# Performance work log

Hardware: AMD Instinct MI355X
Metric: run time of the kernel (lower is better)

Reference implementation:

```python
import jax, jax.numpy as jnp
import numpy as np

B, S, D, H = 4, 2048, 512, 4
HD = D // H
EPS = 1e-5


def layer_norm(x, gamma, beta):
    mu = jnp.mean(x, axis=-1, keepdims=True)
    var = jnp.mean(jnp.square(x - mu), axis=-1, keepdims=True)
    return (x - mu) * jax.lax.rsqrt(var + EPS) * gamma + beta


def setup_inputs() -> dict:
    key = jax.random.key(0)
    ks = jax.random.split(key, 16)
    s_in = 1.0 / np.sqrt(D)
    s_ex = 1.0 / np.sqrt(2 * D)
    return {
        "input_states": jax.random.normal(ks[0], (B, S, D), jnp.float32),
        "positions": jax.random.normal(ks[1], (B, S, 3), jnp.float32),
        "W_expand": jax.random.uniform(ks[2], (D, 2 * D), jnp.float32, -s_in, s_in),
        "b_expand": jax.random.uniform(ks[3], (2 * D,), jnp.float32, -s_in, s_in),
        "W_squeeze": jax.random.uniform(ks[4], (2 * D, D), jnp.float32, -s_ex, s_ex),
        "b_squeeze": jax.random.uniform(ks[5], (D,), jnp.float32, -s_ex, s_ex),
        "gamma": jnp.ones((D,), jnp.float32),
        "beta": jnp.zeros((D,), jnp.float32),
        "Wq": jax.random.uniform(ks[6], (D, D), jnp.float32, -s_in, s_in),
        "bq": jax.random.uniform(ks[7], (D,), jnp.float32, -s_in, s_in),
        "Wk": jax.random.uniform(ks[8], (D, D), jnp.float32, -s_in, s_in),
        "bk": jax.random.uniform(ks[9], (D,), jnp.float32, -s_in, s_in),
        "Wv": jax.random.uniform(ks[10], (D, D), jnp.float32, -s_in, s_in),
        "bv": jax.random.uniform(ks[11], (D,), jnp.float32, -s_in, s_in),
        "alpha": jnp.float32(0.1),
    }


def reference(input_states, positions, W_expand, b_expand, W_squeeze, b_squeeze,
              gamma, beta, Wq, bq, Wk, bk, Wv, bv, alpha):
    # FFN (expand -> relu -> squeeze) + residual + LayerNorm
    h = jax.nn.relu(input_states @ W_expand + b_expand)
    squeezed = h @ W_squeeze + b_squeeze
    se = layer_norm(input_states + squeezed, gamma, beta)

    # q/k/v projections, split heads: [B,H,S,HD]
    q = (se @ Wq + bq).reshape(B, S, H, HD).transpose(0, 2, 1, 3)
    k = (se @ Wk + bk).reshape(B, S, H, HD).transpose(0, 2, 1, 3)
    v = (se @ Wv + bv).reshape(B, S, H, HD).transpose(0, 2, 1, 3)

    scores = jnp.einsum('bhid,bhjd->bhij', q, k) / np.sqrt(HD)

    # squared pairwise distance bias: ||pi||^2 + ||pj||^2 - 2 pi.pj, broadcast over heads
    sq = jnp.sum(positions * positions, axis=-1)  # [B,S]
    dist2 = sq[:, :, None] + sq[:, None, :] - 2.0 * jnp.einsum('bic,bjc->bij', positions, positions)
    dist2 = jnp.maximum(dist2, 0.0)
    scores = scores - alpha * dist2[:, None, :, :]

    w = jax.nn.softmax(scores, axis=-1)
    ctx = jnp.einsum('bhij,bhjd->bhid', w, v)
    ctx = ctx.transpose(0, 2, 1, 3).reshape(B, S, D)

    # same LayerNorm params reused (self.norm applied twice in original)
    return layer_norm(se + ctx, gamma, beta)
```

## Files before the change

kernel.cpp:

```cpp
#include <hip/hip_runtime.h>

typedef __bf16 bf16_t;
typedef __attribute__((ext_vector_type(8))) __bf16 bf16x8;
typedef __attribute__((ext_vector_type(4))) __bf16 bf16x4;
typedef __attribute__((ext_vector_type(4))) float f32x4;
typedef __attribute__((ext_vector_type(16))) float f32x16;

constexpr int Bc = 4, Sc = 2048, Dc = 512, Hc = 4, HDc = 128;
constexpr int Mrows = Bc * Sc;

__device__ inline void gl2lds(const void* g, void* l) {
  __builtin_amdgcn_global_load_lds(
      (__attribute__((address_space(1))) void*)g,
      (__attribute__((address_space(3))) void*)l, 16, 0, 0);
}

__global__ __launch_bounds__(256) void prep_k(
    const float* __restrict__ X, bf16_t* __restrict__ xb,
    const float* __restrict__ We, bf16_t* __restrict__ wtE,
    const float* __restrict__ Ws, bf16_t* __restrict__ wtS,
    const float* __restrict__ Wq, const float* __restrict__ Wk,
    const float* __restrict__ Wv, bf16_t* __restrict__ wtQKV) {
  const int bid = blockIdx.x;
  if (bid < 2048) {
    const long i = ((long)bid * 256 + threadIdx.x) * 8;
    const float4 a = *(const float4*)(X + i);
    const float4 c = *(const float4*)(X + i + 4);
    bf16x8 o;
    o[0] = (bf16_t)a.x; o[1] = (bf16_t)a.y; o[2] = (bf16_t)a.z; o[3] = (bf16_t)a.w;
    o[4] = (bf16_t)c.x; o[5] = (bf16_t)c.y; o[6] = (bf16_t)c.z; o[7] = (bf16_t)c.w;
    *(bf16x8*)(xb + i) = o;
    return;
  }
  __shared__ float tile[32][33];
  const float* src; bf16_t* dst; int K, N, local;
  if (bid < 2560)      { src = We; dst = wtE; K = 512;  N = 1024; local = bid - 2048; }
  else if (bid < 3072) { src = Ws; dst = wtS; K = 1024; N = 512;  local = bid - 2560; }
  else if (bid < 3328) { src = Wq; dst = wtQKV;          K = 512; N = 512; local = bid - 3072; }
  else if (bid < 3584) { src = Wk; dst = wtQKV + 262144; K = 512; N = 512; local = bid - 3328; }
  else                 { src = Wv; dst = wtQKV + 524288; K = 512; N = 512; local = bid - 3584; }
  const int nb = N / 32;
  const int n0 = (local % nb) * 32, k0 = (local / nb) * 32;
  const int tx = threadIdx.x & 31, ty = threadIdx.x >> 5;
#pragma unroll
  for (int i = 0; i < 4; i++)
    tile[ty + i * 8][tx] = src[(long)(k0 + ty + i * 8) * N + n0 + tx];
  __syncthreads();
#pragma unroll
  for (int i = 0; i < 4; i++)
    dst[(long)(n0 + ty + i * 8) * K + k0 + tx] = (bf16_t)tile[tx][ty + i * 8];
}

__global__ __launch_bounds__(256) void pospack_k(const float* __restrict__ pos,
                                                 const float* __restrict__ alphap,
                                                 float* __restrict__ pos2) {
  const float aL = alphap[0] * 1.4426950408889634f;
  const int i = blockIdx.x * 256 + threadIdx.x;
  const float x = pos[(long)i * 3], y = pos[(long)i * 3 + 1], z = pos[(long)i * 3 + 2];
  float4 o; o.x = x; o.y = y; o.z = z; o.w = -aL * (x * x + y * y + z * z);
  *(float4*)(pos2 + (long)i * 4) = o;
}

template <int OMODE, int TN>
__global__ __launch_bounds__(256, 3) void gemm128_k(
    const bf16_t* __restrict__ A, const bf16_t* __restrict__ Bt,
    const float* __restrict__ bias0, const float* __restrict__ bias1,
    const float* __restrict__ bias2, void* __restrict__ out0,
    void* __restrict__ out1, void* __restrict__ out2, int N, int K) {
  __shared__ bf16_t As[128 * 64];
  __shared__ bf16_t Bs[TN * 64];
  constexpr int MT = (TN == 128) ? 4 : 2;
  constexpr int BI = (TN == 128) ? 4 : 2;
  constexpr int MW = (TN == 128) ? 64 : 32;
  const int t = threadIdx.x;
  const int n0 = blockIdx.x * TN, m0 = blockIdx.y * 128;
  const int lane = t & 63, wave = t >> 6;
  const int quad = lane >> 4, ln = lane & 15;
  const int wm = (TN == 128) ? (wave >> 1) : wave;
  const int wn = (TN == 128) ? (wave & 1) : 0;
  const int l8 = lane >> 3, g = lane & 7;
  const bf16_t* aseg = A + (long)(m0 + wave * 32 + l8) * K + g * 8;
  const bf16_t* bseg = Bt + (long)(n0 + wave * (BI * 8) + l8) * K + g * 8;
  bf16_t* asl = &As[(wave * 32) * 64];
  bf16_t* bsl = &Bs[(wave * BI * 8) * 64];
  f32x4 acc[MT][4] = {};
  for (int k0 = 0; k0 < K; k0 += 64) {
#pragma unroll
    for (int i = 0; i < 4; i++)
      gl2lds(aseg + (long)i * 8 * K + k0, asl + i * 8 * 64);
#pragma unroll
    for (int i = 0; i < BI; i++)
      gl2lds(bseg + (long)i * 8 * K + k0, bsl + i * 8 * 64);
    __syncthreads();
#pragma unroll
    for (int kc = 0; kc < 2; kc++) {
      bf16x8 af[MT], bfr[4];
#pragma unroll
      for (int mt = 0; mt < MT; mt++)
        af[mt] = *(const bf16x8*)&As[(wm * MW + mt * 16 + ln) * 64 + kc * 32 + quad * 8];
#pragma unroll
      for (int nt = 0; nt < 4; nt++)
        bfr[nt] = *(const bf16x8*)&Bs[(wn * 64 + nt * 16 + ln) * 64 + kc * 32 + quad * 8];
#pragma unroll
      for (int mt = 0; mt < MT; mt++)
#pragma unroll
        for (int nt = 0; nt < 4; nt++)
          acc[mt][nt] = __builtin_amdgcn_mfma_f32_16x16x32_bf16(af[mt], bfr[nt],
                                                                acc[mt][nt], 0, 0, 0);
    }
    __syncthreads();
  }
#pragma unroll
  for (int nt = 0; nt < 4; nt++) {
    const int gcol = n0 + wn * 64 + nt * 16 + ln;
    if constexpr (OMODE == 0 || OMODE == 1) {
      const float bv = bias0[gcol];
      bf16_t* o = (bf16_t*)out0;
#pragma unroll
      for (int mt = 0; mt < MT; mt++)
#pragma unroll
        for (int r = 0; r < 4; r++) {
          const int grow = m0 + wm * MW + mt * 16 + quad * 4 + r;
          float vv = acc[mt][nt][r] + bv;
          if constexpr (OMODE == 0) vv = vv > 0.f ? vv : 0.f;
          o[(long)grow * N + gcol] = (bf16_t)vv;
        }
    } else {
      const int which = gcol >> 9, n = gcol & 511;
      const int hh = n >> 7, hd = n & 127;
      const float bv = (which == 0 ? bias0 : which == 1 ? bias1 : bias2)[n];
      bf16_t* o = (bf16_t*)(which == 0 ? out0 : which == 1 ? out1 : out2);
#pragma unroll
      for (int mt = 0; mt < MT; mt++)
#pragma unroll
        for (int r = 0; r < 4; r++) {
          const int grow = m0 + wm * MW + mt * 16 + quad * 4 + r;
          const int b = grow >> 11, s = grow & 2047;
          const float vv = acc[mt][nt][r] + bv;
          long idx;
          if (which == 0) {
            idx = ((long)((b * Hc + hh) * Sc + s)) * HDc + hd;
          } else if (which == 1) {
            const int tt = s >> 6, kh = (s >> 5) & 1, key = s & 31;
            const int c = hd >> 4, lk = key + 32 * ((hd >> 3) & 1), j = hd & 7;
            idx = ((((long)((b * Hc + hh) * 32 + tt) * 2 + kh) * 8 + c) * 64 + lk) * 8 + j;
          } else {
            const int tt = s >> 6, ht2 = hd >> 5, kc = (s & 63) >> 4;
            const int lk = (hd & 31) + 32 * ((s >> 3) & 1), j = s & 7;
            idx = ((((long)((b * Hc + hh) * 32 + tt) * 4 + ht2) * 4 + kc) * 64 + lk) * 8 + j;
          }
          o[idx] = (bf16_t)vv;
        }
    }
  }
}

template <int DUAL>
__global__ __launch_bounds__(256) void ln_k(const float* __restrict__ xa,
                                            const bf16_t* __restrict__ xb,
                                            const float* __restrict__ gamma,
                                            const float* __restrict__ beta,
                                            float* __restrict__ out,
                                            bf16_t* __restrict__ outb) {
  const int wave = threadIdx.x >> 6, lane = threadIdx.x & 63;
  const long row = (long)blockIdx.x * 4 + wave;
  const float* a = xa + row * Dc;
  const bf16_t* bp = xb + row * Dc;
  float vv[8];
  float s = 0.f, s2 = 0.f;
#pragma unroll
  for (int i = 0; i < 2; i++) {
    const float4 va = *(const float4*)(a + lane * 4 + i * 256);
    const bf16x4 vb = *(const bf16x4*)(bp + lane * 4 + i * 256);
    const float xs[4] = {va.x, va.y, va.z, va.w};
#pragma unroll
    for (int j = 0; j < 4; j++) {
      const float x = xs[j] + (float)vb[j];
      vv[i * 4 + j] = x;
      s += x;
      s2 += x * x;
    }
  }
#pragma unroll
  for (int off = 1; off < 64; off <<= 1) {
    s += __shfl_xor(s, off, 64);
    s2 += __shfl_xor(s2, off, 64);
  }
  const float mu = s * (1.f / Dc);
  const float var = s2 * (1.f / Dc) - mu * mu;
  const float rstd = rsqrtf(var + 1e-5f);
#pragma unroll
  for (int i = 0; i < 2; i++)
#pragma unroll
    for (int j = 0; j < 4; j++) {
      const int col = lane * 4 + i * 256 + j;
      const float o = (vv[i * 4 + j] - mu) * rstd * gamma[col] + beta[col];
      out[row * Dc + col] = o;
      if constexpr (DUAL) outb[row * Dc + col] = (bf16_t)o;
    }
}

__global__ __launch_bounds__(256, 2) void attn_k(const bf16_t* __restrict__ q,
                                                 const bf16_t* __restrict__ Kg,
                                                 const bf16_t* __restrict__ Vg,
                                                 const float* __restrict__ pos2,
                                                 const float* __restrict__ alphap,
                                                 bf16_t* __restrict__ ctx) {
  __shared__ bf16_t Ks[2][8192];
  __shared__ bf16_t Vts[2][8192];
  __shared__ float pk4[2][64][4];
  __shared__ bf16_t Ps[4][1024];
  __shared__ float RsD[4][32];
  const int t = threadIdx.x;
  const int qt = blockIdx.x, h = blockIdx.y, b = blockIdx.z;
  const int q0 = qt * 64;
  const int wave = t >> 6, lane = t & 63;
  const int l31 = lane & 31, hb = lane >> 5;
  const int rh = wave & 1, kh = wave >> 1;
  const float l2e = 1.4426950408889634f;
  const float scale_l2 = l2e * 0.08838834764831845f;
  const float aL = alphap[0] * l2e;

  bf16x8 qf[8];
  const long qrow = (long)((b * Hc + h) * Sc + q0 + rh * 32 + l31);
#pragma unroll
  for (int c = 0; c < 8; c++)
    qf[c] = *(const bf16x8*)(q + qrow * HDc + c * 16 + hb * 8);
  float pqx, pqy, pqz;
  {
    const float4 p = *(const float4*)(pos2 + (long)(b * Sc + q0 + rh * 32 + l31) * 4);
    pqx = 2.f * aL * p.x; pqy = 2.f * aL * p.y; pqz = 2.f * aL * p.z;
  }

  const bf16_t* ktile = Kg + (long)((b * Hc + h) * 32) * 8192 + lane * 8;
  const bf16_t* vtile = Vg + (long)((b * Hc + h) * 32) * 8192 + lane * 8;
  const float* pcur = pos2 + (long)b * Sc * 4 + lane * 4;
  auto stage = [&](int buf) {
#pragma unroll
    for (int i = 0; i < 4; i++)
      gl2lds(ktile + (wave * 4 + i) * 512, &Ks[buf][(wave * 4 + i) * 512]);
#pragma unroll
    for (int i = 0; i < 4; i++)
      gl2lds(vtile + (wave * 4 + i) * 512, &Vts[buf][(wave * 4 + i) * 512]);
    if (wave == 0) gl2lds(pcur, &pk4[buf][0][0]);
  };
  stage(0);
  ktile += 8192; vtile += 8192; pcur += 256;

  float rsl = 0.f;
  f32x16 accT[4] = {};
  bf16_t* pwbase = &Ps[wave][l31 * 8 + 4 * hb];

  for (int kt = 0; kt < Sc / 64; kt++) {
    const int cur = kt & 1;
    __syncthreads();
    if (kt < Sc / 64 - 1) {
      stage(1 - cur);
      ktile += 8192; vtile += 8192; pcur += 256;
    }
    f32x16 sacc = {};
#pragma unroll
    for (int c = 0; c < 8; c++) {
      const bf16x8 kf = *(const bf16x8*)&Ks[cur][(kh * 8 + c) * 512 + lane * 8];
      sacc = __builtin_amdgcn_mfma_f32_32x32x16_bf16(kf, qf[c], sacc, 0, 0, 0);
    }
#pragma unroll
    for (int g2 = 0; g2 < 4; g2++)
#pragma unroll
      for (int r0 = 0; r0 < 4; r0++) {
        const int kp = r0 + 4 * hb + 8 * g2;
        const float4 pv = *(const float4*)&pk4[cur][kh * 32 + kp][0];
        const float bias = __builtin_fmaf(pqx, pv.x,
                           __builtin_fmaf(pqy, pv.y,
                           __builtin_fmaf(pqz, pv.z, pv.w)));
        const float p = __builtin_amdgcn_exp2f(
            __builtin_fmaf(sacc[g2 * 4 + r0], scale_l2, bias));
        rsl += p;
        pwbase[(g2 >> 1) * 512 + (g2 & 1) * 256 + r0] = (bf16_t)p;
      }
    const bf16x8 pf0 = *(const bf16x8*)&Ps[wave][lane * 8];
    const bf16x8 pf1 = *(const bf16x8*)&Ps[wave][512 + lane * 8];
#pragma unroll
    for (int ht = 0; ht < 4; ht++) {
      const bf16x8 v0 = *(const bf16x8*)&Vts[cur][(ht * 4 + kh * 2 + 0) * 512 + lane * 8];
      accT[ht] = __builtin_amdgcn_mfma_f32_32x32x16_bf16(v0, pf0, accT[ht], 0, 0, 0);
      const bf16x8 v1 = *(const bf16x8*)&Vts[cur][(ht * 4 + kh * 2 + 1) * 512 + lane * 8];
      accT[ht] = __builtin_amdgcn_mfma_f32_32x32x16_bf16(v1, pf1, accT[ht], 0, 0, 0);
    }
  }
  __syncthreads();

  rsl += __shfl_xor(rsl, 32, 64);
  if (hb == 0) RsD[wave][l31] = rsl;
  float* Oc = (float*)&Ks[0][0];
  if (kh == 1) {
#pragma unroll
    for (int ht = 0; ht < 4; ht++)
#pragma unroll
      for (int r = 0; r < 16; r++) {
        const int hdp = (r & 3) + 8 * (r >> 2) + 4 * hb;
        Oc[(ht * 32 + hdp) * 64 + rh * 32 + l31] = accT[ht][r];
      }
  }
  __syncthreads();
  if (kh == 0) {
    const float rinv = 1.f / (RsD[wave][l31] + RsD[wave + 2][l31]);
    const long orow = (long)(b * Sc + q0 + rh * 32 + l31);
#pragma unroll
    for (int ht = 0; ht < 4; ht++)
#pragma unroll
      for (int g2 = 0; g2 < 4; g2++) {
        bf16x4 ov;
#pragma unroll
        for (int r0 = 0; r0 < 4; r0++) {
          const int hdp = r0 + 8 * g2 + 4 * hb;
          ov[r0] = (bf16_t)((accT[ht][g2 * 4 + r0] +
                             Oc[(ht * 32 + hdp) * 64 + rh * 32 + l31]) * rinv);
        }
        *(bf16x4*)(ctx + orow * Dc + h * HDc + ht * 32 + 8 * g2 + 4 * hb) = ov;
      }
  }
}

constexpr size_t SE_OFF = 0;
constexpr size_t SQB_OFF = 16777216;
constexpr size_t SEB_OFF = 25165824;
constexpr size_t Q_OFF = 33554432;
constexpr size_t K_OFF = 41943040;
constexpr size_t V_OFF = 50331648;
constexpr size_t XB_OFF = Q_OFF;
constexpr size_t H_OFF = K_OFF;
constexpr size_t POS2_OFF = SEB_OFF;
constexpr size_t WTE_OFF = 58720256;
constexpr size_t WTS_OFF = WTE_OFF + 1048576;
constexpr size_t WTQKV_OFF = WTS_OFF + 1048576;

extern "C" void kernel_launch(void* const* d_in, const int* in_sizes, int n_in,
                              void* d_out, int out_size, void* d_ws, size_t ws_size,
                              hipStream_t stream) {
  const float* X = (const float*)d_in[0];
  const float* pos = (const float*)d_in[1];
  const float* W_expand = (const float*)d_in[2];
  const float* b_expand = (const float*)d_in[3];
  const float* W_squeeze = (const float*)d_in[4];
  const float* b_squeeze = (const float*)d_in[5];
  const float* gamma = (const float*)d_in[6];
  const float* beta = (const float*)d_in[7];
  const float* Wq = (const float*)d_in[8];
  const float* bq = (const float*)d_in[9];
  const float* Wk = (const float*)d_in[10];
  const float* bk = (const float*)d_in[11];
  const float* Wv = (const float*)d_in[12];
  const float* bv = (const float*)d_in[13];
  const float* alphap = (const float*)d_in[14];

  char* ws = (char*)d_ws;
  float* se = (float*)(ws + SE_OFF);
  bf16_t* sqb = (bf16_t*)(ws + SQB_OFF);
  bf16_t* ctxb = (bf16_t*)(ws + SQB_OFF);
  bf16_t* seb = (bf16_t*)(ws + SEB_OFF);
  float* pos2 = (float*)(ws + POS2_OFF);
  bf16_t* qb = (bf16_t*)(ws + Q_OFF);
  bf16_t* kb = (bf16_t*)(ws + K_OFF);
  bf16_t* vb = (bf16_t*)(ws + V_OFF);
  bf16_t* xbb = (bf16_t*)(ws + XB_OFF);
  bf16_t* hb = (bf16_t*)(ws + H_OFF);
  bf16_t* wtE = (bf16_t*)(ws + WTE_OFF);
  bf16_t* wtS = (bf16_t*)(ws + WTS_OFF);
  bf16_t* wtQKV = (bf16_t*)(ws + WTQKV_OFF);

  prep_k<<<3840, 256, 0, stream>>>(X, xbb, W_expand, wtE, W_squeeze, wtS,
                                   Wq, Wk, Wv, wtQKV);
  gemm128_k<0, 128><<<dim3(1024 / 128, Mrows / 128), 256, 0, stream>>>(
      xbb, wtE, b_expand, nullptr, nullptr, hb, nullptr, nullptr, 1024, 512);
  gemm128_k<1, 64><<<dim3(512 / 64, Mrows / 128), 256, 0, stream>>>(
      hb, wtS, b_squeeze, nullptr, nullptr, sqb, nullptr, nullptr, 512, 1024);
  ln_k<1><<<Mrows / 4, 256, 0, stream>>>(X, sqb, gamma, beta, se, seb);
  gemm128_k<2, 128><<<dim3(1536 / 128, Mrows / 128), 256, 0, stream>>>(
      seb, wtQKV, bq, bk, bv, qb, kb, vb, 1536, 512);
  pospack_k<<<Mrows / 256, 256, 0, stream>>>(pos, alphap, pos2);
  attn_k<<<dim3(Sc / 64, Hc, Bc), 256, 0, stream>>>(qb, kb, vb, pos2, alphap, ctxb);
  ln_k<0><<<Mrows / 4, 256, 0, stream>>>(se, ctxb, gamma, beta, (float*)d_out, nullptr);

  (void)in_sizes; (void)n_in; (void)out_size; (void)ws_size;
}
```

Measured before the change: 235.7 us.

## Double-buffer LDS tiles with XOR swizzle in bf16 GEMM kernel

The GEMM main loop now uses two LDS buffers per operand. It issues global-to-LDS loads for the next K tile right after the barrier, so they overlap with the MFMA work on the current tile, and it drops the trailing barrier. The global column chunk is XOR-swizzled with the row index when staged, and the fragment reads undo the swizzle to cut LDS bank conflicts. The doubled LDS use lowers the occupancy hint for the TN=128 variant from 3 to 2 blocks per CU, which may reduce latency hiding.

```diff
diff --git a/kernel.cpp b/kernel.cpp
--- a/kernel.cpp
+++ b/kernel.cpp
@@ -62,13 +62,13 @@
 }
 
 template <int OMODE, int TN>
-__global__ __launch_bounds__(256, 3) void gemm128_k(
+__global__ __launch_bounds__(256, (TN == 128) ? 2 : 3) void gemm128_k(
     const bf16_t* __restrict__ A, const bf16_t* __restrict__ Bt,
     const float* __restrict__ bias0, const float* __restrict__ bias1,
     const float* __restrict__ bias2, void* __restrict__ out0,
     void* __restrict__ out1, void* __restrict__ out2, int N, int K) {
-  __shared__ bf16_t As[128 * 64];
-  __shared__ bf16_t Bs[TN * 64];
+  __shared__ bf16_t As[2][128 * 64];
+  __shared__ bf16_t Bs[2][TN * 64];
   constexpr int MT = (TN == 128) ? 4 : 2;
   constexpr int BI = (TN == 128) ? 4 : 2;
   constexpr int MW = (TN == 128) ? 64 : 32;
@@ -79,28 +79,34 @@
   const int wm = (TN == 128) ? (wave >> 1) : wave;
   const int wn = (TN == 128) ? (wave & 1) : 0;
   const int l8 = lane >> 3, g = lane & 7;
-  const bf16_t* aseg = A + (long)(m0 + wave * 32 + l8) * K + g * 8;
-  const bf16_t* bseg = Bt + (long)(n0 + wave * (BI * 8) + l8) * K + g * 8;
-  bf16_t* asl = &As[(wave * 32) * 64];
-  bf16_t* bsl = &Bs[(wave * BI * 8) * 64];
+  const bf16_t* aseg = A + (long)(m0 + wave * 32 + l8) * K + (g ^ l8) * 8;
+  const bf16_t* bseg = Bt + (long)(n0 + wave * (BI * 8) + l8) * K + (g ^ l8) * 8;
+  auto stage = [&](int buf, int k0) {
+#pragma unroll
+    for (int i = 0; i < 4; i++)
+      gl2lds(aseg + (long)i * 8 * K + k0, &As[buf][(wave * 32 + i * 8) * 64]);
+#pragma unroll
+    for (int i = 0; i < BI; i++)
+      gl2lds(bseg + (long)i * 8 * K + k0, &Bs[buf][(wave * BI * 8 + i * 8) * 64]);
+  };
   f32x4 acc[MT][4] = {};
-  for (int k0 = 0; k0 < K; k0 += 64) {
-#pragma unroll
-    for (int i = 0; i < 4; i++)
-      gl2lds(aseg + (long)i * 8 * K + k0, asl + i * 8 * 64);
-#pragma unroll
-    for (int i = 0; i < BI; i++)
-      gl2lds(bseg + (long)i * 8 * K + k0, bsl + i * 8 * 64);
+  stage(0, 0);
+  const int niter = K / 64;
+  for (int it = 0; it < niter; it++) {
+    const int cur = it & 1;
     __syncthreads();
+    if (it + 1 < niter) stage(1 - cur, (it + 1) * 64);
 #pragma unroll
     for (int kc = 0; kc < 2; kc++) {
       bf16x8 af[MT], bfr[4];
 #pragma unroll
       for (int mt = 0; mt < MT; mt++)
-        af[mt] = *(const bf16x8*)&As[(wm * MW + mt * 16 + ln) * 64 + kc * 32 + quad * 8];
+        af[mt] = *(const bf16x8*)&As[cur][(wm * MW + mt * 16 + ln) * 64 +
+                                          (((kc * 4 + quad) ^ (ln & 7)) * 8)];
 #pragma unroll
       for (int nt = 0; nt < 4; nt++)
-        bfr[nt] = *(const bf16x8*)&Bs[(wn * 64 + nt * 16 + ln) * 64 + kc * 32 + quad * 8];
+        bfr[nt] = *(const bf16x8*)&Bs[cur][(wn * 64 + nt * 16 + ln) * 64 +
+                                           (((kc * 4 + quad) ^ (ln & 7)) * 8)];
 #pragma unroll
       for (int mt = 0; mt < MT; mt++)
 #pragma unroll
@@ -108,7 +114,6 @@
           acc[mt][nt] = __builtin_amdgcn_mfma_f32_16x16x32_bf16(af[mt], bfr[nt],
                                                                 acc[mt][nt], 0, 0, 0);
     }
-    __syncthreads();
   }
 #pragma unroll
   for (int nt = 0; nt < 4; nt++) {
```

Measured after the change: 233.5 us. Within noise of the previous version (-0.9%).
